# Kernel optimization log

Measured on AMD Instinct MI355X. Metric: run time of the kernel, lower is better.

Reference implementation:

```python
import jax, jax.numpy as jnp
import numpy as np

IN_DIM = 512

def setup_inputs() -> dict:
    key = jax.random.key(0)
    ks = jax.random.split(key, 7)
    s = 1.0 / np.sqrt(IN_DIM)
    x = jax.random.normal(ks[0], (8, 2048, IN_DIM), dtype=jnp.float32)
    Wq = jax.random.uniform(ks[1], (IN_DIM, IN_DIM), jnp.float32, -s, s)
    bq = jax.random.uniform(ks[2], (IN_DIM,), jnp.float32, -s, s)
    Wk = jax.random.uniform(ks[3], (IN_DIM, IN_DIM), jnp.float32, -s, s)
    bk = jax.random.uniform(ks[4], (IN_DIM,), jnp.float32, -s, s)
    Wv = jax.random.uniform(ks[5], (IN_DIM, IN_DIM), jnp.float32, -s, s)
    bv = jax.random.uniform(ks[6], (IN_DIM,), jnp.float32, -s, s)
    return {"x": x, "Wq": Wq, "bq": bq, "Wk": Wk, "bk": bk, "Wv": Wv, "bv": bv}

def reference(x, Wq, bq, Wk, bk, Wv, bv):
    # Q,K,V projections: torch Linear is x @ W.T + b; Wq here is [out,in]
    q = jnp.einsum('bsc,dc->bsd', x, Wq) + bq
    k = jnp.einsum('bsc,dc->bsd', x, Wk) + bk
    v = jnp.einsum('bsc,dc->bsd', x, Wv) + bv
    energy = jnp.einsum('bqd,bkd->bqk', q, k)  # no scaling, matches source
    attention = jax.nn.softmax(energy, axis=-1)
    out = jnp.einsum('bqk,bkd->bqd', attention, v)
    return out
```

## Files before the change

### kernel.cpp

```cpp
#include <hip/hip_runtime.h>

typedef unsigned short u16;
typedef _Float16 f16;

using half8   = __attribute__((ext_vector_type(8))) _Float16;
using f32x4   = __attribute__((ext_vector_type(4))) float;
using ushort8 = __attribute__((ext_vector_type(8))) unsigned short;
using us4     = __attribute__((ext_vector_type(4))) unsigned short;
using float4v = __attribute__((ext_vector_type(4))) float;

#define B_  8
#define S_  2048
#define D_  512

__device__ __forceinline__ u16 f2h(float f) {
  f16 h = (f16)f;
  u16 u;
  __builtin_memcpy(&u, &h, 2);
  return u;
}

__device__ __forceinline__ float h2f(u16 h) {
  f16 x;
  __builtin_memcpy(&x, &h, 2);
  return (float)x;
}

__device__ __forceinline__ void stage16(const void* g, void* l) {
  __builtin_amdgcn_global_load_lds((const __attribute__((address_space(1))) void*)g,
                                   (__attribute__((address_space(3))) void*)l,
                                   16, 0, 0);
}

__device__ __forceinline__ void xcd_remap(int& bx, int& by, int& bz) {
  const int lin = ((int)blockIdx.z * (int)gridDim.y + (int)blockIdx.y) * (int)gridDim.x
                  + (int)blockIdx.x;
  const int nwg = (int)gridDim.x * (int)gridDim.y * (int)gridDim.z;
  const int swz = (lin & 7) * (nwg >> 3) + (lin >> 3);
  bx = swz % (int)gridDim.x;
  const int tmp = swz / (int)gridDim.x;
  by = tmp % (int)gridDim.y;
  bz = tmp / (int)gridDim.y;
}

__device__ __forceinline__ void gemm128(const u16* __restrict__ A, const u16* __restrict__ B,
                                        int K, int m0, int n0,
                                        u16* lds, f32x4 acc[4][4]) {
  constexpr int TILE_ELEMS = 4096;
  constexpr int BUF_ELEMS  = 8192;
  const int tid  = threadIdx.x;
  const int lane = tid & 63;
  const int wave = tid >> 6;
  const int wr = wave >> 1, wc = wave & 1;
  const int fr   = lane & 15;
  const int fgrp = lane >> 4;

  int sr[2], sc[2];
  #pragma unroll
  for (int s = 0; s < 2; ++s) {
    const int p    = tid * 16 + s * 4096;
    const int R    = p >> 7;
    const int slot = (p >> 4) & 7;
    const int s0   = slot ^ (R & 7);
    sr[s] = 2 * R + (s0 >> 2);
    sc[s] = (s0 & 3) * 8;
  }

  int offA[4], offB[4];
  #pragma unroll
  for (int m = 0; m < 4; ++m) {
    const int ra = wr * 64 + m * 16 + fr;
    const int Ra = ra >> 1;
    offA[m] = Ra * 128 + (((((ra & 1) << 2) | fgrp) ^ (Ra & 7)) << 4);
    const int rb = wc * 64 + m * 16 + fr;
    const int Rb = rb >> 1;
    offB[m] = Rb * 128 + (((((rb & 1) << 2) | fgrp) ^ (Rb & 7)) << 4);
  }

  const f32x4 vzero = {0.f, 0.f, 0.f, 0.f};
  #pragma unroll
  for (int m = 0; m < 4; ++m)
    #pragma unroll
    for (int n = 0; n < 4; ++n)
      acc[m][n] = vzero;

  const int T = K / 32;

  auto STAGE = [&](int t, u16* buf) {
    #pragma unroll
    for (int s = 0; s < 2; ++s) {
      stage16(A + (size_t)(m0 + sr[s]) * K + t * 32 + sc[s],
              buf + s * 2048 + wave * 512);
      stage16(B + (size_t)(n0 + sr[s]) * K + t * 32 + sc[s],
              buf + TILE_ELEMS + s * 2048 + wave * 512);
    }
  };

  STAGE(0, lds);
  STAGE(1, lds + BUF_ELEMS);

  int r = 0;
  for (int u = 0; u < T; ++u) {
    if (u + 1 < T) {
      asm volatile("s_waitcnt vmcnt(4)\n\ts_barrier" ::: "memory");
    } else {
      asm volatile("s_waitcnt vmcnt(0)\n\ts_barrier" ::: "memory");
    }
    const u16* buf = lds + r * BUF_ELEMS;
    half8 a[4], b[4];
    #pragma unroll
    for (int m = 0; m < 4; ++m)
      a[m] = *(const half8*)((const char*)buf + offA[m]);
    #pragma unroll
    for (int n = 0; n < 4; ++n)
      b[n] = *(const half8*)((const char*)(buf + TILE_ELEMS) + offB[n]);
    if (u + 2 < T)
      STAGE(u + 2, lds + (r == 0 ? 2 : r - 1) * BUF_ELEMS);
    __builtin_amdgcn_s_setprio(1);
    #pragma unroll
    for (int m = 0; m < 4; ++m)
      #pragma unroll
      for (int n = 0; n < 4; ++n)
        acc[m][n] = __builtin_amdgcn_mfma_f32_16x16x32_f16(a[m], b[n], acc[m][n], 0, 0, 0);
    __builtin_amdgcn_s_setprio(0);
    r = (r == 2) ? 0 : r + 1;
  }
}

template<int M_REP>
__device__ __forceinline__ void core8p(const u16* __restrict__ A,
                                       const u16* __restrict__ B,
                                       int K, int m0, int n0,
                                       u16* lds, f32x4 acc[M_REP][4]) {
  constexpr int M2   = M_REP / 2;
  constexpr int BM   = M_REP * 32;
  constexpr int AIS  = BM * 32;
  constexpr int BOFF = BM * 64;
  constexpr int BUFE = BM * 64 + 16384;
  constexpr int ASL  = BM / 128;
  constexpr int L    = 2 * ASL + 4;
  constexpr int QSRA = (BM == 256) ? 32 : 16;

  const int tid  = threadIdx.x;
  const int lane = tid & 63;
  const int wave = tid >> 6;
  const int wr = wave >> 2, wc = wave & 3;
  const int fr = lane & 15, fgrp = lane >> 4;

  int    dstA[2][ASL];  size_t gA[2][ASL];
  int    dstB[2][2];    size_t gB[2][2];
  #pragma unroll
  for (int q = 0; q < 2; ++q) {
    #pragma unroll
    for (int s = 0; s < ASL; ++s) {
      int ks, jr;
      if constexpr (ASL == 2) { ks = s; jr = wave * 8; }
      else                    { ks = wave >> 2; jr = (wave & 3) * 8; }
      const int R   = (jr / QSRA) * (2 * QSRA) + q * QSRA + (jr % QSRA);
      const int dst = ks * AIS + R * 64;
      dstA[q][s] = dst;
      const int e   = dst + lane * 8;
      const int ks2 = e / AIS, le = e - ks2 * AIS;
      const int RR  = le >> 6;
      const int s0  = ((le >> 3) & 7) ^ (RR & 7);
      gA[q][s] = (size_t)(m0 + 2 * RR + (s0 >> 2)) * K + ks2 * 32 + (s0 & 3) * 8;
    }
    #pragma unroll
    for (int s = 0; s < 2; ++s) {
      const int jr  = wave * 8;
      const int R   = (jr / 16) * 32 + q * 16 + (jr % 16);
      const int dst = BOFF + s * 8192 + R * 64;
      dstB[q][s] = dst;
      const int e   = dst - BOFF + lane * 8;
      const int ks2 = e / 8192, le = e - ks2 * 8192;
      const int RR  = le >> 6;
      const int s0  = ((le >> 3) & 7) ^ (RR & 7);
      gB[q][s] = (size_t)(n0 + 2 * RR + (s0 >> 2)) * K + ks2 * 32 + (s0 & 3) * 8;
    }
  }

  int offA[2][M2][2], offB[2][2][2];
  #pragma unroll
  for (int mh = 0; mh < 2; ++mh)
    #pragma unroll
    for (int m = 0; m < M2; ++m)
      #pragma unroll
      for (int ks = 0; ks < 2; ++ks) {
        const int ra = wr * (M_REP * 16) + (mh * M2 + m) * 16 + fr;
        const int Ra = ra >> 1;
        offA[mh][m][ks] = (ks * AIS + Ra * 64) * 2 +
                          (((((ra & 1) << 2) | fgrp) ^ (Ra & 7)) << 4);
      }
  #pragma unroll
  for (int nh = 0; nh < 2; ++nh)
    #pragma unroll
    for (int n = 0; n < 2; ++n)
      #pragma unroll
      for (int ks = 0; ks < 2; ++ks) {
        const int rb = wc * 64 + (nh * 2 + n) * 16 + fr;
        const int Rb = rb >> 1;
        offB[nh][n][ks] = (BOFF + ks * 8192 + Rb * 64) * 2 +
                          (((((rb & 1) << 2) | fgrp) ^ (Rb & 7)) << 4);
      }

  const f32x4 vzero = {0.f, 0.f, 0.f, 0.f};
  #pragma unroll
  for (int m = 0; m < M_REP; ++m)
    #pragma unroll
    for (int n = 0; n < 4; ++n)
      acc[m][n] = vzero;

  const int NT = K >> 6;

  auto stageA = [&](int q, int tt) {
    u16* bb = lds + (tt & 1) * BUFE;
    #pragma unroll
    for (int s = 0; s < ASL; ++s)
      stage16(A + gA[q][s] + (size_t)tt * 64, bb + dstA[q][s]);
  };
  auto stageB = [&](int q, int tt) {
    u16* bb = lds + (tt & 1) * BUFE;
    #pragma unroll
    for (int s = 0; s < 2; ++s)
      stage16(B + gB[q][s] + (size_t)tt * 64, bb + dstB[q][s]);
  };

  stageA(0, 0); stageB(0, 0); stageB(1, 0); stageA(1, 0);
  stageA(0, 1); stageB(0, 1); stageB(1, 1); stageA(1, 1);

  half8 a[M2][2], blo[2][2], bhi[2][2];

#define MFMA_Q(MH, BB, NB)                                                       \
  __builtin_amdgcn_s_setprio(1);                                                 \
  _Pragma("unroll")                                                              \
  for (int m = 0; m < M2; ++m)                                                   \
    _Pragma("unroll")                                                            \
    for (int n = 0; n < 2; ++n)                                                  \
      _Pragma("unroll")                                                          \
      for (int ks = 0; ks < 2; ++ks)                                             \
        acc[(MH) * M2 + m][(NB) + n] = __builtin_amdgcn_mfma_f32_16x16x32_f16(   \
            a[m][ks], BB[n][ks], acc[(MH) * M2 + m][(NB) + n], 0, 0, 0);         \
  __builtin_amdgcn_s_setprio(0);

  for (int t = 0; t < NT; ++t) {
    const char* rb_ = (const char*)(lds + (t & 1) * BUFE);
    const int tt = t + 2;
    const bool st = (tt < NT);

    if (t == NT - 1) asm volatile("s_waitcnt vmcnt(0)\n\ts_barrier" ::: "memory");
    else if constexpr (L == 8) asm volatile("s_waitcnt vmcnt(8)\n\ts_barrier" ::: "memory");
    else                       asm volatile("s_waitcnt vmcnt(6)\n\ts_barrier" ::: "memory");
    #pragma unroll
    for (int m = 0; m < M2; ++m)
      #pragma unroll
      for (int ks = 0; ks < 2; ++ks)
        a[m][ks] = *(const half8*)(rb_ + offA[0][m][ks]);
    #pragma unroll
    for (int n = 0; n < 2; ++n)
      #pragma unroll
      for (int ks = 0; ks < 2; ++ks)
        blo[n][ks] = *(const half8*)(rb_ + offB[0][n][ks]);
    MFMA_Q(0, blo, 0)
    asm volatile("s_barrier" ::: "memory");

    #pragma unroll
    for (int n = 0; n < 2; ++n)
      #pragma unroll
      for (int ks = 0; ks < 2; ++ks)
        bhi[n][ks] = *(const half8*)(rb_ + offB[1][n][ks]);
    if (st) { stageA(0, tt); stageB(0, tt); }
    asm volatile("s_barrier" ::: "memory");
    MFMA_Q(0, bhi, 2)
    asm volatile("s_barrier" ::: "memory");

    #pragma unroll
    for (int m = 0; m < M2; ++m)
      #pragma unroll
      for (int ks = 0; ks < 2; ++ks)
        a[m][ks] = *(const half8*)(rb_ + offA[1][m][ks]);
    if (st) stageB(1, tt);
    asm volatile("s_barrier" ::: "memory");
    MFMA_Q(1, bhi, 2)
    asm volatile("s_barrier" ::: "memory");

    if (st) stageA(1, tt);
    asm volatile("s_barrier" ::: "memory");
    MFMA_Q(1, blo, 0)
    asm volatile("s_barrier" ::: "memory");
  }
#undef MFMA_Q
}

__global__ __launch_bounds__(256) void proj_kernel(
    const u16* __restrict__ xh, const u16* __restrict__ Wh,
    const float* __restrict__ bq, const float* __restrict__ bk, const float* __restrict__ bv,
    u16* __restrict__ Qb, u16* __restrict__ Kb, u16* __restrict__ Vt) {
  __shared__ __align__(16) u16 lds[3 * 8192];
  int bx, by, bz;
  xcd_remap(bx, by, bz);
  const int z  = bz;
  const int m0 = by * 128;
  const int n0 = bx * 128;
  const u16* W = Wh + (size_t)z * D_ * D_;
  const float* bias = (z == 0) ? bq : (z == 1) ? bk : bv;
  f32x4 acc[4][4];
  gemm128(xh, W, D_, m0, n0, lds, acc);

  const int lane = threadIdx.x & 63;
  const int wave = threadIdx.x >> 6;
  const int wr = wave >> 1, wc = wave & 1;
  #pragma unroll
  for (int m = 0; m < 4; ++m) {
    const int gr0 = m0 + wr * 64 + m * 16 + ((lane >> 4) << 2);
    #pragma unroll
    for (int n = 0; n < 4; ++n) {
      const int gc = n0 + wc * 64 + n * 16 + (lane & 15);
      const float bb = bias[gc];
      if (z < 2) {
        u16* O = z ? Kb : Qb;
        #pragma unroll
        for (int r = 0; r < 4; ++r)
          O[(size_t)(gr0 + r) * D_ + gc] = f2h(acc[m][n][r] + bb);
      } else {
        const int bidx = gr0 >> 11;
        const int s    = gr0 & 2047;
        us4 p;
        #pragma unroll
        for (int r = 0; r < 4; ++r) p[r] = f2h(acc[m][n][r] + bb);
        *(us4*)(Vt + ((size_t)bidx * D_ + gc) * S_ + s) = p;
      }
    }
  }
}

__global__ __launch_bounds__(512, 1) void qk_kernel(
    const u16* __restrict__ Qb, const u16* __restrict__ Kb, u16* __restrict__ E,
    size_t sA, size_t sE) {
  __shared__ __align__(16) u16 lds[2 * (256 * 64 + 16384)];
  int bx, by, bz;
  xcd_remap(bx, by, bz);
  const int z  = bz;
  const int m0 = by * 256;
  const int n0 = bx * 256;
  f32x4 acc[8][4];
  core8p<8>(Qb + (size_t)z * sA, Kb + (size_t)z * sA, D_, m0, n0, lds, acc);

  u16* Eb = E + (size_t)z * sE;
  const int lane = threadIdx.x & 63;
  const int wave = threadIdx.x >> 6;
  const int wr = wave >> 2, wc = wave & 3;
  #pragma unroll
  for (int m = 0; m < 8; ++m) {
    const int gr0 = m0 + wr * 128 + m * 16 + ((lane >> 4) << 2);
    #pragma unroll
    for (int n = 0; n < 4; ++n) {
      const int gc = n0 + wc * 64 + n * 16 + (lane & 15);
      #pragma unroll
      for (int r = 0; r < 4; ++r)
        Eb[(size_t)(gr0 + r) * S_ + gc] = f2h(acc[m][n][r]);
    }
  }
}

__global__ __launch_bounds__(256) void softmax_kernel(u16* __restrict__ E) {
  const int row  = blockIdx.x * 4 + (threadIdx.x >> 6);
  const int lane = threadIdx.x & 63;
  u16* R = E + (size_t)row * S_;
  float e[32];
  #pragma unroll
  for (int i = 0; i < 4; ++i) {
    ushort8 v = *(const ushort8*)(R + i * 512 + lane * 8);
    #pragma unroll
    for (int j = 0; j < 8; ++j) e[i * 8 + j] = h2f(v[j]);
  }
  float m = e[0];
  #pragma unroll
  for (int i = 1; i < 32; ++i) m = fmaxf(m, e[i]);
  for (int off = 32; off > 0; off >>= 1) m = fmaxf(m, __shfl_xor(m, off, 64));
  float s = 0.f;
  #pragma unroll
  for (int i = 0; i < 32; ++i) { e[i] = __expf(e[i] - m); s += e[i]; }
  for (int off = 32; off > 0; off >>= 1) s += __shfl_xor(s, off, 64);
  const float inv = 1.f / s;
  #pragma unroll
  for (int i = 0; i < 4; ++i) {
    ushort8 v;
    #pragma unroll
    for (int j = 0; j < 8; ++j) v[j] = f2h(e[i * 8 + j] * inv);
    *(ushort8*)(R + i * 512 + lane * 8) = v;
  }
}

__global__ __launch_bounds__(512, 1) void pv_kernel(
    const u16* __restrict__ P, const u16* __restrict__ Vt, float* __restrict__ out,
    size_t sP, size_t sV, size_t sO) {
  __shared__ __align__(16) u16 lds[2 * (128 * 64 + 16384)];
  int bx, by, bz;
  xcd_remap(bx, by, bz);
  const int z  = bz;
  const int m0 = by * 128;
  const int n0 = bx * 256;
  f32x4 acc[4][4];
  core8p<4>(P + (size_t)z * sP, Vt + (size_t)z * sV, S_, m0, n0, lds, acc);

  float* Ob = out + (size_t)z * sO;
  const int lane = threadIdx.x & 63;
  const int wave = threadIdx.x >> 6;
  const int wr = wave >> 2, wc = wave & 3;
  #pragma unroll
  for (int m = 0; m < 4; ++m) {
    const int gr0 = m0 + wr * 64 + m * 16 + ((lane >> 4) << 2);
    #pragma unroll
    for (int n = 0; n < 4; ++n) {
      const int gc = n0 + wc * 64 + n * 16 + (lane & 15);
      #pragma unroll
      for (int r = 0; r < 4; ++r)
        Ob[(size_t)(gr0 + r) * D_ + gc] = acc[m][n][r];
    }
  }
}

__global__ __launch_bounds__(256) void cvt_kernel(const float* __restrict__ in,
                                                  u16* __restrict__ out, int n8) {
  const int i = blockIdx.x * 256 + threadIdx.x;
  if (i >= n8) return;
  const float4v a = *(const float4v*)(in + (size_t)i * 8);
  const float4v b = *(const float4v*)(in + (size_t)i * 8 + 4);
  ushort8 o;
  o[0] = f2h(a[0]); o[1] = f2h(a[1]); o[2] = f2h(a[2]); o[3] = f2h(a[3]);
  o[4] = f2h(b[0]); o[5] = f2h(b[1]); o[6] = f2h(b[2]); o[7] = f2h(b[3]);
  *(ushort8*)(out + (size_t)i * 8) = o;
}

__global__ __launch_bounds__(256) void cvt3_kernel(const float* __restrict__ w0,
                                                   const float* __restrict__ w1,
                                                   const float* __restrict__ w2,
                                                   u16* __restrict__ out, int n8) {
  const int i = blockIdx.x * 256 + threadIdx.x;
  if (i >= n8) return;
  const float* in = (blockIdx.y == 0) ? w0 : (blockIdx.y == 1) ? w1 : w2;
  u16* o_ = out + (size_t)blockIdx.y * D_ * D_;
  const float4v a = *(const float4v*)(in + (size_t)i * 8);
  const float4v b = *(const float4v*)(in + (size_t)i * 8 + 4);
  ushort8 o;
  o[0] = f2h(a[0]); o[1] = f2h(a[1]); o[2] = f2h(a[2]); o[3] = f2h(a[3]);
  o[4] = f2h(b[0]); o[5] = f2h(b[1]); o[6] = f2h(b[2]); o[7] = f2h(b[3]);
  *(ushort8*)(o_ + (size_t)i * 8) = o;
}

extern "C" void kernel_launch(void* const* d_in, const int* in_sizes, int n_in,
                              void* d_out, int out_size, void* d_ws, size_t ws_size,
                              hipStream_t stream) {
  (void)in_sizes; (void)n_in; (void)out_size;
  const float* x  = (const float*)d_in[0];
  const float* Wq = (const float*)d_in[1];
  const float* bq = (const float*)d_in[2];
  const float* Wk = (const float*)d_in[3];
  const float* bk = (const float*)d_in[4];
  const float* Wv = (const float*)d_in[5];
  const float* bv = (const float*)d_in[6];
  float* out = (float*)d_out;

  char* ws = (char*)d_ws;
  size_t off = 0;
  auto alloc = [&](size_t bytes) -> char* {
    char* p = ws + off;
    off += (bytes + 255) & ~(size_t)255;
    return p;
  };
  const size_t MS = (size_t)B_ * S_;
  u16* xh = (u16*)alloc(MS * D_ * 2);
  u16* Wh = (u16*)alloc(3ull * D_ * D_ * 2);
  u16* Qb = (u16*)alloc(MS * D_ * 2);
  u16* Kb = (u16*)alloc(MS * D_ * 2);
  u16* Vt = (u16*)alloc(MS * D_ * 2);
  const size_t Efull = (size_t)B_ * S_ * S_ * 2;
  const bool full = ws_size >= off + Efull;
  u16* E = (u16*)alloc(full ? Efull : (size_t)S_ * S_ * 2);

  {
    const int n8 = (int)(MS * D_ / 8);
    cvt_kernel<<<dim3((n8 + 255) / 256), dim3(256), 0, stream>>>(x, xh, n8);
    const int w8 = D_ * D_ / 8;
    cvt3_kernel<<<dim3((w8 + 255) / 256, 3), dim3(256), 0, stream>>>(Wq, Wk, Wv, Wh, w8);
  }

  proj_kernel<<<dim3(D_ / 128, MS / 128, 3), dim3(256), 0, stream>>>(
      xh, Wh, bq, bk, bv, Qb, Kb, Vt);

  if (full) {
    qk_kernel<<<dim3(S_ / 256, S_ / 256, B_), dim3(512), 0, stream>>>(
        Qb, Kb, E, (size_t)S_ * D_, (size_t)S_ * S_);
    softmax_kernel<<<dim3(B_ * S_ / 4), dim3(256), 0, stream>>>(E);
    pv_kernel<<<dim3(D_ / 256, S_ / 128, B_), dim3(512), 0, stream>>>(
        E, Vt, out, (size_t)S_ * S_, (size_t)D_ * S_, (size_t)S_ * D_);
  } else {
    for (int b = 0; b < B_; ++b) {
      qk_kernel<<<dim3(S_ / 256, S_ / 256, 1), dim3(512), 0, stream>>>(
          Qb + (size_t)b * S_ * D_, Kb + (size_t)b * S_ * D_, E, 0, 0);
      softmax_kernel<<<dim3(S_ / 4), dim3(256), 0, stream>>>(E);
      pv_kernel<<<dim3(D_ / 256, S_ / 128, 1), dim3(512), 0, stream>>>(
          E, Vt + (size_t)b * D_ * S_, out + (size_t)b * S_ * D_, 0, 0, 0);
    }
  }
}
```

Measured before the change: 156.9 us.

## Restructure GEMM main loop from 8-phase to 2-phase barrier schedule

```diff
diff --git a/kernel.cpp b/kernel.cpp
--- a/kernel.cpp
+++ b/kernel.cpp
@@ -128,7 +128,7 @@
 }
 
 template<int M_REP>
-__device__ __forceinline__ void core8p(const u16* __restrict__ A,
+__device__ __forceinline__ void core2p(const u16* __restrict__ A,
                                        const u16* __restrict__ B,
                                        int K, int m0, int n0,
                                        u16* lds, f32x4 acc[M_REP][4]) {
@@ -138,7 +138,6 @@
   constexpr int BOFF = BM * 64;
   constexpr int BUFE = BM * 64 + 16384;
   constexpr int ASL  = BM / 128;
-  constexpr int L    = 2 * ASL + 4;
   constexpr int QSRA = (BM == 256) ? 32 : 16;
 
   const int tid  = threadIdx.x;
@@ -226,12 +225,11 @@
   };
 
   stageA(0, 0); stageB(0, 0); stageB(1, 0); stageA(1, 0);
-  stageA(0, 1); stageB(0, 1); stageB(1, 1); stageA(1, 1);
+  stageA(0, 1); stageB(0, 1); stageB(1, 1);
 
   half8 a[M2][2], blo[2][2], bhi[2][2];
 
 #define MFMA_Q(MH, BB, NB)                                                       \
-  __builtin_amdgcn_s_setprio(1);                                                 \
   _Pragma("unroll")                                                              \
   for (int m = 0; m < M2; ++m)                                                   \
     _Pragma("unroll")                                                            \
@@ -239,17 +237,16 @@
       _Pragma("unroll")                                                          \
       for (int ks = 0; ks < 2; ++ks)                                             \
         acc[(MH) * M2 + m][(NB) + n] = __builtin_amdgcn_mfma_f32_16x16x32_f16(   \
-            a[m][ks], BB[n][ks], acc[(MH) * M2 + m][(NB) + n], 0, 0, 0);         \
-  __builtin_amdgcn_s_setprio(0);
+            a[m][ks], BB[n][ks], acc[(MH) * M2 + m][(NB) + n], 0, 0, 0);
 
   for (int t = 0; t < NT; ++t) {
     const char* rb_ = (const char*)(lds + (t & 1) * BUFE);
-    const int tt = t + 2;
-    const bool st = (tt < NT);
-
-    if (t == NT - 1) asm volatile("s_waitcnt vmcnt(0)\n\ts_barrier" ::: "memory");
-    else if constexpr (L == 8) asm volatile("s_waitcnt vmcnt(8)\n\ts_barrier" ::: "memory");
-    else                       asm volatile("s_waitcnt vmcnt(6)\n\ts_barrier" ::: "memory");
+
+    if (t == NT - 1)           asm volatile("s_waitcnt vmcnt(0)\n\ts_barrier" ::: "memory");
+    else if constexpr (ASL == 2) asm volatile("s_waitcnt vmcnt(6)\n\ts_barrier" ::: "memory");
+    else                       asm volatile("s_waitcnt vmcnt(5)\n\ts_barrier" ::: "memory");
+
+    if (t + 1 < NT) stageA(1, t + 1);
     #pragma unroll
     for (int m = 0; m < M2; ++m)
       #pragma unroll
@@ -258,35 +255,30 @@
     #pragma unroll
     for (int n = 0; n < 2; ++n)
       #pragma unroll
-      for (int ks = 0; ks < 2; ++ks)
+      for (int ks = 0; ks < 2; ++ks) {
         blo[n][ks] = *(const half8*)(rb_ + offB[0][n][ks]);
+        bhi[n][ks] = *(const half8*)(rb_ + offB[1][n][ks]);
+      }
+    asm volatile("s_waitcnt lgkmcnt(0)" ::: "memory");
+    __builtin_amdgcn_sched_barrier(0);
+    __builtin_amdgcn_s_setprio(1);
     MFMA_Q(0, blo, 0)
+    MFMA_Q(0, bhi, 2)
+    __builtin_amdgcn_s_setprio(0);
     asm volatile("s_barrier" ::: "memory");
 
-    #pragma unroll
-    for (int n = 0; n < 2; ++n)
-      #pragma unroll
-      for (int ks = 0; ks < 2; ++ks)
-        bhi[n][ks] = *(const half8*)(rb_ + offB[1][n][ks]);
-    if (st) { stageA(0, tt); stageB(0, tt); }
-    asm volatile("s_barrier" ::: "memory");
-    MFMA_Q(0, bhi, 2)
-    asm volatile("s_barrier" ::: "memory");
-
+    if (t + 2 < NT) { stageA(0, t + 2); stageB(0, t + 2); stageB(1, t + 2); }
     #pragma unroll
     for (int m = 0; m < M2; ++m)
       #pragma unroll
       for (int ks = 0; ks < 2; ++ks)
         a[m][ks] = *(const half8*)(rb_ + offA[1][m][ks]);
-    if (st) stageB(1, tt);
-    asm volatile("s_barrier" ::: "memory");
+    asm volatile("s_waitcnt lgkmcnt(0)" ::: "memory");
+    __builtin_amdgcn_sched_barrier(0);
+    __builtin_amdgcn_s_setprio(1);
     MFMA_Q(1, bhi, 2)
-    asm volatile("s_barrier" ::: "memory");
-
-    if (st) stageA(1, tt);
-    asm volatile("s_barrier" ::: "memory");
     MFMA_Q(1, blo, 0)
-    asm volatile("s_barrier" ::: "memory");
+    __builtin_amdgcn_s_setprio(0);
   }
 #undef MFMA_Q
 }
@@ -343,7 +335,7 @@
   const int m0 = by * 256;
   const int n0 = bx * 256;
   f32x4 acc[8][4];
-  core8p<8>(Qb + (size_t)z * sA, Kb + (size_t)z * sA, D_, m0, n0, lds, acc);
+  core2p<8>(Qb + (size_t)z * sA, Kb + (size_t)z * sA, D_, m0, n0, lds, acc);
 
   u16* Eb = E + (size_t)z * sE;
   const int lane = threadIdx.x & 63;
@@ -401,7 +393,7 @@
   const int m0 = by * 128;
   const int n0 = bx * 256;
   f32x4 acc[4][4];
-  core8p<4>(P + (size_t)z * sP, Vt + (size_t)z * sV, S_, m0, n0, lds, acc);
+  core2p<4>(P + (size_t)z * sP, Vt + (size_t)z * sV, S_, m0, n0, lds, acc);
 
   float* Ob = out + (size_t)z * sO;
   const int lane = threadIdx.x & 63;
```

New measurement: 158.8 us. Within noise of the previous version (+1.2%).

## Restructure 8-wave GEMM mainloop to prefetch next tile fragments during MFMA

Applied to the files above, without the earlier changes.

```diff
diff --git a/kernel.cpp b/kernel.cpp
--- a/kernel.cpp
+++ b/kernel.cpp
@@ -12,6 +12,9 @@
 #define B_  8
 #define S_  2048
 #define D_  512
+
+#define VMCNT(N)  asm volatile("s_waitcnt vmcnt(" #N ")" ::: "memory")
+#define SBAR()    asm volatile("s_barrier" ::: "memory")
 
 __device__ __forceinline__ u16 f2h(float f) {
   f16 h = (f16)f;
@@ -128,17 +131,16 @@
 }
 
 template<int M_REP>
-__device__ __forceinline__ void core8p(const u16* __restrict__ A,
-                                       const u16* __restrict__ B,
-                                       int K, int m0, int n0,
-                                       u16* lds, f32x4 acc[M_REP][4]) {
+__device__ __forceinline__ void core4ra(const u16* __restrict__ A,
+                                        const u16* __restrict__ B,
+                                        int K, int m0, int n0,
+                                        u16* lds, f32x4 acc[M_REP][4]) {
   constexpr int M2   = M_REP / 2;
   constexpr int BM   = M_REP * 32;
   constexpr int AIS  = BM * 32;
   constexpr int BOFF = BM * 64;
   constexpr int BUFE = BM * 64 + 16384;
   constexpr int ASL  = BM / 128;
-  constexpr int L    = 2 * ASL + 4;
   constexpr int QSRA = (BM == 256) ? 32 : 16;
 
   const int tid  = threadIdx.x;
@@ -228,9 +230,26 @@
   stageA(0, 0); stageB(0, 0); stageB(1, 0); stageA(1, 0);
   stageA(0, 1); stageB(0, 1); stageB(1, 1); stageA(1, 1);
 
-  half8 a[M2][2], blo[2][2], bhi[2][2];
-
-#define MFMA_Q(MH, BB, NB)                                                       \
+  half8 a0[M2][2], a1[M2][2], blo[2][2], bhi[2][2];
+
+  if constexpr (ASL == 2) VMCNT(12); else VMCNT(9);
+  SBAR();
+  {
+    const char* rb0 = (const char*)lds;
+    #pragma unroll
+    for (int m = 0; m < M2; ++m)
+      #pragma unroll
+      for (int ks = 0; ks < 2; ++ks)
+        a0[m][ks] = *(const half8*)(rb0 + offA[0][m][ks]);
+    #pragma unroll
+    for (int n = 0; n < 2; ++n)
+      #pragma unroll
+      for (int ks = 0; ks < 2; ++ks)
+        blo[n][ks] = *(const half8*)(rb0 + offB[0][n][ks]);
+  }
+  if constexpr (ASL == 2) VMCNT(10); else VMCNT(7);
+
+#define MFMA_Q(AA, BB, MH, NB)                                                   \
   __builtin_amdgcn_s_setprio(1);                                                 \
   _Pragma("unroll")                                                              \
   for (int m = 0; m < M2; ++m)                                                   \
@@ -239,54 +258,60 @@
       _Pragma("unroll")                                                          \
       for (int ks = 0; ks < 2; ++ks)                                             \
         acc[(MH) * M2 + m][(NB) + n] = __builtin_amdgcn_mfma_f32_16x16x32_f16(   \
-            a[m][ks], BB[n][ks], acc[(MH) * M2 + m][(NB) + n], 0, 0, 0);         \
+            AA[m][ks], BB[n][ks], acc[(MH) * M2 + m][(NB) + n], 0, 0, 0);        \
   __builtin_amdgcn_s_setprio(0);
 
   for (int t = 0; t < NT; ++t) {
-    const char* rb_ = (const char*)(lds + (t & 1) * BUFE);
-    const int tt = t + 2;
-    const bool st = (tt < NT);
-
-    if (t == NT - 1) asm volatile("s_waitcnt vmcnt(0)\n\ts_barrier" ::: "memory");
-    else if constexpr (L == 8) asm volatile("s_waitcnt vmcnt(8)\n\ts_barrier" ::: "memory");
-    else                       asm volatile("s_waitcnt vmcnt(6)\n\ts_barrier" ::: "memory");
-    #pragma unroll
-    for (int m = 0; m < M2; ++m)
-      #pragma unroll
-      for (int ks = 0; ks < 2; ++ks)
-        a[m][ks] = *(const half8*)(rb_ + offA[0][m][ks]);
-    #pragma unroll
-    for (int n = 0; n < 2; ++n)
-      #pragma unroll
-      for (int ks = 0; ks < 2; ++ks)
-        blo[n][ks] = *(const half8*)(rb_ + offB[0][n][ks]);
-    MFMA_Q(0, blo, 0)
-    asm volatile("s_barrier" ::: "memory");
-
+    const char* rb_  = (const char*)(lds + (t & 1) * BUFE);
+    const char* rbn_ = (const char*)(lds + ((t + 1) & 1) * BUFE);
+
+    SBAR();
+    MFMA_Q(a0, blo, 0, 0)
     #pragma unroll
     for (int n = 0; n < 2; ++n)
       #pragma unroll
       for (int ks = 0; ks < 2; ++ks)
         bhi[n][ks] = *(const half8*)(rb_ + offB[1][n][ks]);
-    if (st) { stageA(0, tt); stageB(0, tt); }
-    asm volatile("s_barrier" ::: "memory");
-    MFMA_Q(0, bhi, 2)
-    asm volatile("s_barrier" ::: "memory");
-
+    if (t == NT - 1) VMCNT(0);
+    else if constexpr (ASL == 2) VMCNT(8); else VMCNT(6);
+
+    SBAR();
+    MFMA_Q(a0, bhi, 0, 2)
     #pragma unroll
     for (int m = 0; m < M2; ++m)
       #pragma unroll
       for (int ks = 0; ks < 2; ++ks)
-        a[m][ks] = *(const half8*)(rb_ + offA[1][m][ks]);
-    if (st) stageB(1, tt);
-    asm volatile("s_barrier" ::: "memory");
-    MFMA_Q(1, bhi, 2)
-    asm volatile("s_barrier" ::: "memory");
-
-    if (st) stageA(1, tt);
-    asm volatile("s_barrier" ::: "memory");
-    MFMA_Q(1, blo, 0)
-    asm volatile("s_barrier" ::: "memory");
+        a1[m][ks] = *(const half8*)(rb_ + offA[1][m][ks]);
+    if (t + 2 < NT) { stageA(0, t + 2); stageB(0, t + 2); }
+
+    SBAR();
+    MFMA_Q(a1, bhi, 1, 2)
+    if (t + 2 < NT) stageB(1, t + 2);
+    if (t + 1 < NT) {
+      if (t + 2 < NT) { if constexpr (ASL == 2) VMCNT(10); else VMCNT(8); }
+      else            { if constexpr (ASL == 2) VMCNT(4);  else VMCNT(3); }
+    }
+
+    SBAR();
+    MFMA_Q(a1, blo, 1, 0)
+    if (t + 1 < NT) {
+      #pragma unroll
+      for (int m = 0; m < M2; ++m)
+        #pragma unroll
+        for (int ks = 0; ks < 2; ++ks)
+          a0[m][ks] = *(const half8*)(rbn_ + offA[0][m][ks]);
+      #pragma unroll
+      for (int n = 0; n < 2; ++n)
+        #pragma unroll
+        for (int ks = 0; ks < 2; ++ks)
+          blo[n][ks] = *(const half8*)(rbn_ + offB[0][n][ks]);
+      if (t + 2 < NT) {
+        stageA(1, t + 2);
+        if constexpr (ASL == 2) VMCNT(10); else VMCNT(7);
+      } else {
+        if constexpr (ASL == 2) VMCNT(2); else VMCNT(1);
+      }
+    }
   }
 #undef MFMA_Q
 }
@@ -343,7 +368,7 @@
   const int m0 = by * 256;
   const int n0 = bx * 256;
   f32x4 acc[8][4];
-  core8p<8>(Qb + (size_t)z * sA, Kb + (size_t)z * sA, D_, m0, n0, lds, acc);
+  core4ra<8>(Qb + (size_t)z * sA, Kb + (size_t)z * sA, D_, m0, n0, lds, acc);
 
   u16* Eb = E + (size_t)z * sE;
   const int lane = threadIdx.x & 63;
@@ -401,7 +426,7 @@
   const int m0 = by * 128;
   const int n0 = bx * 256;
   f32x4 acc[4][4];
-  core8p<4>(P + (size_t)z * sP, Vt + (size_t)z * sV, S_, m0, n0, lds, acc);
+  core4ra<4>(P + (size_t)z * sP, Vt + (size_t)z * sV, S_, m0, n0, lds, acc);
 
   float* Ob = out + (size_t)z * sO;
   const int lane = threadIdx.x & 63;
```

New measurement: 156.0 us (median of 2 runs). Within noise of the previous version (-0.6%).
